# Kernel optimization log

Hardware: AMD Instinct MI355X
Metric: run time of the kernel (lower is better)

The kernel has to match this reference:

```python
import jax, jax.numpy as jnp
import numpy as np

B, K, D = 4096, 100, 64          # batch, multi_factor*top_k, emb_dim
NU, NI = 100000, 50000           # n_users, n_items
MLP_DIMS = [2 * K, K, K // 2, 25, 12, 1]  # 200,100,50,25,12,1


def setup_inputs() -> dict:
    key = jax.random.key(0)
    ks = jax.random.split(key, 30)
    inp = {
        "user_idxs": jax.random.randint(ks[0], (B,), 0, NU),
        "item_idxs": jax.random.randint(ks[1], (B,), 0, NI),
        "user_idx_tensor": jax.random.randint(ks[2], (NU, K), 0, NU),
        "item_idx_tensor": jax.random.randint(ks[3], (NI, K), 0, NI),
        "user_scr_tensor": jax.random.uniform(ks[4], (NU, K), dtype=jnp.float32),
        "item_scr_tensor": jax.random.uniform(ks[5], (NI, K), dtype=jnp.float32),
        "user_emb": jax.random.normal(ks[6], (NU, D), dtype=jnp.float32),
        "item_emb": jax.random.normal(ks[7], (NI, D), dtype=jnp.float32),
    }
    i = 8
    for net in ("n1", "n2"):
        for li, (a, b) in enumerate(zip(MLP_DIMS[:-1], MLP_DIMS[1:]), 1):
            lim = 1.0 / np.sqrt(a)
            inp[f"{net}_w{li}"] = jax.random.uniform(ks[i], (a, b), minval=-lim, maxval=lim, dtype=jnp.float32); i += 1
            inp[f"{net}_b{li}"] = jax.random.uniform(ks[i], (b,), minval=-lim, maxval=lim, dtype=jnp.float32); i += 1
    return inp


def _mlp(x, ws, bs):
    for w, b in zip(ws[:-1], bs[:-1]):
        x = jax.nn.relu(x @ w + b)
    return x @ ws[-1] + bs[-1]


def reference(user_idxs, item_idxs, user_idx_tensor, item_idx_tensor,
              user_scr_tensor, item_scr_tensor, user_emb, item_emb,
              n1_w1, n1_b1, n1_w2, n1_b2, n1_w3, n1_b3, n1_w4, n1_b4, n1_w5, n1_b5,
              n2_w1, n2_b1, n2_w2, n2_b2, n2_w3, n2_b3, n2_w4, n2_b4, n2_w5, n2_b5):
    # neighbor gather: [B,K,D] embeddings and [B,K] scores
    u_e = user_emb[user_idx_tensor[user_idxs]]
    u_s = user_scr_tensor[user_idxs]
    i_e = item_emb[item_idx_tensor[item_idxs]]
    i_s = item_scr_tensor[item_idxs]
    # torch bmm(emb [B,K,D], score[:,None,:].repeat(1,D,1) [B,D,K]) -> [B,K,K];
    # since the repeated score matrix has identical rows, result = emb.sum(-1) (x) score
    su = u_e.sum(-1)[:, :, None] * u_s[:, None, :]  # [B,K,K]
    si = i_e.sum(-1)[:, :, None] * i_s[:, None, :]  # [B,K,K]
    # cat(dim=1).permute(0,2,1) == cat of transposes along last dim
    x1 = jnp.concatenate([su.transpose(0, 2, 1), si.transpose(0, 2, 1)], axis=2)  # [B,K,2K]
    x2 = jnp.concatenate([su, si], axis=2)                                        # [B,K,2K]
    ws1 = [n1_w1, n1_w2, n1_w3, n1_w4, n1_w5]; bs1 = [n1_b1, n1_b2, n1_b3, n1_b4, n1_b5]
    ws2 = [n2_w1, n2_w2, n2_w3, n2_w4, n2_w5]; bs2 = [n2_b1, n2_b2, n2_b3, n2_b4, n2_b5]
    c1 = _mlp(x1, ws1, bs1)[..., 0]  # [B,K]
    c2 = _mlp(x2, ws2, bs2)[..., 0]  # [B,K]
    return jax.nn.sigmoid(jnp.mean(c1 + c2, axis=1))  # [B]
```

## Files before the change

kernel.cpp:

```cpp
#include <hip/hip_runtime.h>
#include <math.h>

#define KDIM 100
#define DDIM 64

typedef __bf16 bf16x8 __attribute__((ext_vector_type(8)));
typedef float  f32x4  __attribute__((ext_vector_type(4)));
typedef float  f32x2  __attribute__((ext_vector_type(2)));
typedef unsigned int u32;
typedef u32 u32x2 __attribute__((ext_vector_type(2)));

struct Weights {
  const float *w1, *b1, *w2, *b2, *w3, *b3, *w4, *b4, *w5, *b5;
};

__device__ __forceinline__ f32x2 vmax2(f32x2 a, f32x2 b) {
#if __has_builtin(__builtin_elementwise_max)
  return __builtin_elementwise_max(a, b);
#else
  return (f32x2){fmaxf(a[0], b[0]), fmaxf(a[1], b[1])};
#endif
}

constexpr int L_VEC  = 0;
constexpr int L_PA   = 400;
constexpr int L_TAIL = 912;
constexpr int L_C    = 1424;
constexpr int SM_F   = 1680;
constexpr int H2T_BYTE = SM_F * 4;
constexpr int H3T_BYTE = H2T_BYTE + 4 * 2048;
constexpr int SM_BYTES = H3T_BYTE + 4 * 1024;

__global__ void prep_kernel(const float* __restrict__ user_emb,
                            const float* __restrict__ item_emb,
                            float* __restrict__ u_rowsum,
                            float* __restrict__ i_rowsum,
                            int NU, int NI, Weights N1, Weights N2,
                            __bf16* __restrict__ wfrag, float* __restrict__ tail) {
  const int tid  = threadIdx.x;
  const int lane = tid & 63;
  const int g = lane >> 4, c16 = lane & 15;
  const int gw = (blockIdx.x * blockDim.x + tid) >> 6;

  if (gw < 42) {
    const int net = gw / 21, f = gw % 21;
    const Weights W = net ? N2 : N1;
    bf16x8 v;
    if (f < 16) {
      const int mt = f >> 2, ks = f & 3;
      #pragma unroll
      for (int i = 0; i < 8; ++i) {
        const int k = 32 * ks + 8 * g + i, m = 16 * mt + c16;
        v[i] = (__bf16)((k < 100 && m < 50) ? W.w2[k * 50 + m] : 0.f);
      }
    } else if (f < 20) {
      const int mt = (f - 16) >> 1, ks = (f - 16) & 1;
      #pragma unroll
      for (int i = 0; i < 8; ++i) {
        const int k = 32 * ks + 8 * g + i, m = 16 * mt + c16;
        v[i] = (__bf16)((k < 50 && m < 25) ? W.w3[k * 25 + m] : 0.f);
      }
    } else {
      #pragma unroll
      for (int i = 0; i < 8; ++i) {
        const int k = 8 * g + i, m = c16;
        v[i] = (__bf16)((k < 25 && m < 12) ? W.w4[k * 12 + m] : 0.f);
      }
    }
    *(bf16x8*)(wfrag + (size_t)gw * 512 + lane * 8) = v;
  }

  if (blockIdx.x == 0) {
    for (int e = tid; e < 512; e += 256) {
      float v;
      if (e < 256)      { const int j = e & 127; const Weights W = (e & 128) ? N2 : N1; v = (j < 100) ? W.b1[j] : 0.f; }
      else if (e < 384) { const int t = e - 256; const int j = t & 63; const Weights W = (t & 64) ? N2 : N1; v = (j < 50) ? W.b2[j] : 0.f; }
      else if (e < 448) { const int t = e - 384; const int j = t & 31; const Weights W = (t & 32) ? N2 : N1; v = (j < 25) ? W.b3[j] : 0.f; }
      else if (e < 480) { const int t = e - 448; const int j = t & 15; const Weights W = (t & 16) ? N2 : N1; v = (j < 12) ? W.b4[j] : 0.f; }
      else              { const int t = e - 480; const int j = t & 15; const Weights W = (t & 16) ? N2 : N1; v = (j < 12) ? W.w5[j] : 0.f; }
      tail[e] = v;
    }
  }

  const int NR = NU + NI;
  const int chunk = lane & 15, lrow = lane >> 4;
  const int nwave = (gridDim.x * blockDim.x) >> 6;
  for (int base = gw * 4; base < NR; base += nwave * 4) {
    const int r = base + lrow;
    float s = 0.f;
    if (r < NR) {
      const float* src = (r < NU) ? (user_emb + (size_t)r * DDIM)
                                  : (item_emb + (size_t)(r - NU) * DDIM);
      const float4 v4 = ((const float4*)src)[chunk];
      s = v4.x + v4.y + v4.z + v4.w;
    }
    s += __shfl_xor(s, 1); s += __shfl_xor(s, 2);
    s += __shfl_xor(s, 4); s += __shfl_xor(s, 8);
    if (chunk == 0 && r < NR) {
      if (r < NU) u_rowsum[r] = s; else i_rowsum[r - NU] = s;
    }
  }
}

__global__ void __launch_bounds__(256) proj_kernel(
    const int* __restrict__ user_idxs, const int* __restrict__ item_idxs,
    const int* __restrict__ uidx_t, const int* __restrict__ iidx_t,
    const float* __restrict__ uscr, const float* __restrict__ iscr,
    const float* __restrict__ u_rowsum, const float* __restrict__ i_rowsum,
    const float* __restrict__ n1w1, const float* __restrict__ n2w1,
    float* __restrict__ VG, float* __restrict__ PAG, int B)
{
  __shared__ float VT[100][20];
  __shared__ float W1S[50][128];
  __shared__ int sidx[16];
  const int tid = threadIdx.x;
  const int sel = blockIdx.x & 3;
  const int b0  = (blockIdx.x >> 2) * 16;

  if (tid < 16) {
    const int b = b0 + tid;
    const int bb = (b < B) ? b : (B - 1);
    sidx[tid] = (sel & 1) ? item_idxs[bb] : user_idxs[bb];
  }
  __syncthreads();

  {
    const int bl = tid >> 4, strip = tid & 15;
    const size_t row = (size_t)sidx[bl] * KDIM;
    if (sel < 2) {
      const int* it = (sel == 0) ? uidx_t : iidx_t;
      const float* rs = (sel == 0) ? u_rowsum : i_rowsum;
      int idxs[7];
      #pragma unroll
      for (int i = 0; i < 7; ++i) {
        const int k = strip + 16 * i;
        idxs[i] = (k < KDIM) ? it[row + k] : 0;
      }
      #pragma unroll
      for (int i = 0; i < 7; ++i) {
        const int k = strip + 16 * i;
        if (k < KDIM) VT[k][bl] = rs[idxs[i]];
      }
    } else {
      const float* sc = (sel == 2) ? uscr : iscr;
      #pragma unroll
      for (int i = 0; i < 7; ++i) {
        const int k = strip + 16 * i;
        if (k < KDIM) VT[k][bl] = sc[row + k];
      }
    }
  }

  const float* w1 = (sel < 2) ? n1w1 : n2w1;
  const int rb = (sel & 1) * KDIM;
  const int jg = tid & 31, bg = tid >> 5;
  float acc[2][4];
  #pragma unroll
  for (int bi = 0; bi < 2; ++bi)
    #pragma unroll
    for (int ji = 0; ji < 4; ++ji) acc[bi][ji] = 0.f;

  for (int kh = 0; kh < 2; ++kh) {
    __syncthreads();
    for (int e = tid; e < 1600; e += 256) {
      const int k = e >> 5, s = e & 31;
      float4 v;
      if (s < 25) v = ((const float4*)(w1 + (size_t)(rb + kh * 50 + k) * KDIM))[s];
      else        v = make_float4(0.f, 0.f, 0.f, 0.f);
      *(float4*)&W1S[k][4 * s] = v;
    }
    __syncthreads();
    #pragma unroll 2
    for (int k = 0; k < 50; ++k) {
      const f32x2 v = *(const f32x2*)&VT[kh * 50 + k][2 * bg];
      const float4 w = *(const float4*)&W1S[k][4 * jg];
      const float ww[4] = {w.x, w.y, w.z, w.w};
      #pragma unroll
      for (int ji = 0; ji < 4; ++ji) {
        acc[0][ji] = fmaf(v[0], ww[ji], acc[0][ji]);
        acc[1][ji] = fmaf(v[1], ww[ji], acc[1][ji]);
      }
    }
  }

  #pragma unroll
  for (int bi = 0; bi < 2; ++bi) {
    const int b = b0 + 2 * bg + bi;
    if (b < B) {
      float4 o = make_float4(acc[bi][0], acc[bi][1], acc[bi][2], acc[bi][3]);
      *(float4*)(PAG + ((size_t)sel * B + b) * 128 + 4 * jg) = o;
    }
  }
  {
    const int bl = tid >> 4, strip = tid & 15;
    const int b = b0 + bl;
    if (b < B) {
      float* dst = VG + ((size_t)sel * B + b) * KDIM;
      #pragma unroll
      for (int i = 0; i < 7; ++i) {
        const int k = strip + 16 * i;
        if (k < KDIM) dst[k] = VT[k][bl];
      }
    }
  }
}

__global__ void __launch_bounds__(256, 4) mlp_kernel(
    const float* __restrict__ VG, const float* __restrict__ PAG,
    const float* __restrict__ tail,
    const float* __restrict__ n1b5, const float* __restrict__ n2b5,
    const __bf16* __restrict__ wfrag, float* __restrict__ out, int B)
{
  __shared__ __align__(16) char smem[SM_BYTES];
  float* sm = (float*)smem;
  const int tid  = threadIdx.x;
  const int lane = tid & 63;
  const int wv   = tid >> 6;
  const int g    = lane >> 4;
  const int c16  = lane & 15;
  const int b    = blockIdx.x;
  const f32x2 Z2 = {0.f, 0.f};

  if (tid < 128) {
    const int sel = tid >> 5, s = tid & 31;
    *(float4*)&sm[L_PA + sel * 128 + 4 * s] =
        *(const float4*)(PAG + ((size_t)sel * B + b) * 128 + 4 * s);
  } else {
    const int t = tid - 128;
    *(float4*)&sm[L_TAIL + 4 * t] = *(const float4*)(tail + 4 * t);
  }
  if (tid < 200) {
    const int sel = tid / 50, r = tid % 50;
    *(f32x2*)&sm[L_VEC + sel * 100 + 2 * r] =
        *(const f32x2*)(VG + ((size_t)sel * B + b) * KDIM + 2 * r);
  }
  __syncthreads();

  const int net = wv >> 1;
  const int qp  = wv & 1;
  const int vA  = net ? (L_VEC + 0)   : (L_VEC + 200);
  const int vB  = net ? (L_VEC + 100) : (L_VEC + 300);
  const int pAo = L_PA + net * 256;
  const int pBo = pAo + 128;
  const char* wfb = (const char*)wfrag + net * 21 * 1024;
  char* h2t = smem + H2T_BYTE + wv * 2048;
  char* h3t = smem + H3T_BYTE + wv * 1024;
  const float b5v = net ? n2b5[0] : n1b5[0];
  const int t7 = c16 & 7, t3 = c16 & 3;

  for (int qq = 0; qq < 2; ++qq) {
    const int q  = 2 * qp + qq;
    const int r0 = 25 * q;

    float sAr[2], sBr[2];
    #pragma unroll
    for (int c = 0; c < 2; ++c) {
      const int row = r0 + 16 * c + c16;
      const int rr = row < KDIM ? row : (KDIM - 1);
      sAr[c] = sm[vA + rr]; sBr[c] = sm[vB + rr];
    }

    f32x4 acc2[2][4];
    #pragma unroll
    for (int c = 0; c < 2; ++c)
      #pragma unroll
      for (int mt = 0; mt < 4; ++mt) acc2[c][mt] = (f32x4){0.f, 0.f, 0.f, 0.f};

    #pragma unroll
    for (int ks = 0; ks < 4; ++ks) {
      const int jb = 32 * ks + 8 * g;
      const f32x2* pa2 = (const f32x2*)&sm[pAo + jb];
      const f32x2* pb2 = (const f32x2*)&sm[pBo + jb];
      const f32x2* b12 = (const f32x2*)&sm[L_TAIL + net * 128 + jb];
      f32x2 paf[4], pbf[4], b1f[4];
      #pragma unroll
      for (int i = 0; i < 4; ++i) { paf[i] = pa2[i]; pbf[i] = pb2[i]; b1f[i] = b12[i]; }
      bf16x8 hb[2];
      #pragma unroll
      for (int c = 0; c < 2; ++c) {
        const f32x2 sa = {sAr[c], sAr[c]}, sb = {sBr[c], sBr[c]};
        bf16x8 a;
        #pragma unroll
        for (int i2 = 0; i2 < 4; ++i2) {
          f32x2 t = sb * pbf[i2] + b1f[i2];
          t = sa * paf[i2] + t;
          t = vmax2(t, Z2);
          a[2 * i2]     = (__bf16)t[0];
          a[2 * i2 + 1] = (__bf16)t[1];
        }
        hb[c] = a;
      }
      __builtin_amdgcn_s_setprio(1);
      #pragma unroll
      for (int mt = 0; mt < 4; ++mt) {
        const bf16x8 a = *(const bf16x8*)(wfb + (mt * 4 + ks) * 1024 + lane * 16);
        acc2[0][mt] = __builtin_amdgcn_mfma_f32_16x16x32_bf16(a, hb[0], acc2[0][mt], 0, 0, 0);
        acc2[1][mt] = __builtin_amdgcn_mfma_f32_16x16x32_bf16(a, hb[1], acc2[1][mt], 0, 0, 0);
      }
      __builtin_amdgcn_s_setprio(0);
    }

    #pragma unroll
    for (int c = 0; c < 2; ++c) {
      #pragma unroll
      for (int mt = 0; mt < 4; ++mt) {
        const f32x2* b2p = (const f32x2*)&sm[L_TAIL + 256 + net * 64 + 16 * mt + 4 * g];
        const f32x4 x = acc2[c][mt];
        const f32x2 lo = vmax2((f32x2){x[0], x[1]} + b2p[0], Z2);
        const f32x2 hi = vmax2((f32x2){x[2], x[3]} + b2p[1], Z2);
        union { __bf16 e[4]; u32x2 w; } o;
        o.e[0] = (__bf16)lo[0]; o.e[1] = (__bf16)lo[1];
        o.e[2] = (__bf16)hi[0]; o.e[3] = (__bf16)hi[1];
        const int S = (2 * mt + (g >> 1)) ^ t7;
        *(u32x2*)(h2t + c16 * 128 + S * 16 + (g & 1) * 8) = o.w;
      }

      f32x4 acc3[2];
      #pragma unroll
      for (int mt = 0; mt < 2; ++mt) acc3[mt] = (f32x4){0.f, 0.f, 0.f, 0.f};
      #pragma unroll
      for (int ks = 0; ks < 2; ++ks) {
        const int S = (4 * ks + g) ^ t7;
        const bf16x8 hbf = *(const bf16x8*)(h2t + c16 * 128 + S * 16);
        __builtin_amdgcn_s_setprio(1);
        #pragma unroll
        for (int mt = 0; mt < 2; ++mt) {
          const bf16x8 a = *(const bf16x8*)(wfb + (16 + mt * 2 + ks) * 1024 + lane * 16);
          acc3[mt] = __builtin_amdgcn_mfma_f32_16x16x32_bf16(a, hbf, acc3[mt], 0, 0, 0);
        }
        __builtin_amdgcn_s_setprio(0);
      }
      #pragma unroll
      for (int mt = 0; mt < 2; ++mt) {
        const f32x2* b3p = (const f32x2*)&sm[L_TAIL + 384 + net * 32 + 16 * mt + 4 * g];
        const f32x4 x = acc3[mt];
        const f32x2 lo = vmax2((f32x2){x[0], x[1]} + b3p[0], Z2);
        const f32x2 hi = vmax2((f32x2){x[2], x[3]} + b3p[1], Z2);
        union { __bf16 e[4]; u32x2 w; } o;
        o.e[0] = (__bf16)lo[0]; o.e[1] = (__bf16)lo[1];
        o.e[2] = (__bf16)hi[0]; o.e[3] = (__bf16)hi[1];
        const int S = (2 * mt + (g >> 1)) ^ t3;
        *(u32x2*)(h3t + c16 * 64 + S * 16 + (g & 1) * 8) = o.w;
      }

      {
        const int S = g ^ t3;
        const bf16x8 hbf = *(const bf16x8*)(h3t + c16 * 64 + S * 16);
        const bf16x8 a = *(const bf16x8*)(wfb + 20 * 1024 + lane * 16);
        const f32x4 z = {0.f, 0.f, 0.f, 0.f};
        __builtin_amdgcn_s_setprio(1);
        const f32x4 acc4 = __builtin_amdgcn_mfma_f32_16x16x32_bf16(a, hbf, z, 0, 0, 0);
        __builtin_amdgcn_s_setprio(0);
        const f32x2* b4p = (const f32x2*)&sm[L_TAIL + 448 + net * 16 + 4 * g];
        const f32x2* w5p = (const f32x2*)&sm[L_TAIL + 480 + net * 16 + 4 * g];
        const f32x2 lo = vmax2((f32x2){acc4[0], acc4[1]} + b4p[0], Z2);
        const f32x2 hi = vmax2((f32x2){acc4[2], acc4[3]} + b4p[1], Z2);
        float v = lo[0] * w5p[0][0] + lo[1] * w5p[0][1]
                + hi[0] * w5p[1][0] + hi[1] * w5p[1][1];
        v += __shfl_xor(v, 16); v += __shfl_xor(v, 32);
        const int lr = 16 * c + c16;
        if (g == 0 && lr < 25)
          sm[L_C + net * 128 + r0 + lr] = v + b5v;
      }
    }
  }
  __syncthreads();

  float v = 0.f;
  if (tid < KDIM) v = sm[L_C + tid] + sm[L_C + 128 + tid];
  if (tid < 128) {
    #pragma unroll
    for (int d = 1; d < 64; d <<= 1) v += __shfl_xor(v, d);
    if ((tid & 63) == 0) sm[tid >> 6] = v;
  }
  __syncthreads();
  if (tid == 0) out[b] = 1.f / (1.f + expf(-0.01f * (sm[0] + sm[1])));
}

extern "C" void kernel_launch(void* const* d_in, const int* in_sizes, int n_in,
                              void* d_out, int out_size, void* d_ws, size_t ws_size,
                              hipStream_t stream) {
  const int*   user_idxs = (const int*)d_in[0];
  const int*   item_idxs = (const int*)d_in[1];
  const int*   uidx_t    = (const int*)d_in[2];
  const int*   iidx_t    = (const int*)d_in[3];
  const float* uscr      = (const float*)d_in[4];
  const float* iscr      = (const float*)d_in[5];
  const float* uemb      = (const float*)d_in[6];
  const float* iemb      = (const float*)d_in[7];

  const int B  = in_sizes[0];
  const int NU = in_sizes[6] / DDIM;
  const int NI = in_sizes[7] / DDIM;

  Weights N1 { (const float*)d_in[8],  (const float*)d_in[9],
               (const float*)d_in[10], (const float*)d_in[11],
               (const float*)d_in[12], (const float*)d_in[13],
               (const float*)d_in[14], (const float*)d_in[15],
               (const float*)d_in[16], (const float*)d_in[17] };
  Weights N2 { (const float*)d_in[18], (const float*)d_in[19],
               (const float*)d_in[20], (const float*)d_in[21],
               (const float*)d_in[22], (const float*)d_in[23],
               (const float*)d_in[24], (const float*)d_in[25],
               (const float*)d_in[26], (const float*)d_in[27] };

  char* ws = (char*)d_ws;
  float* u_rowsum = (float*)ws;
  float* i_rowsum = u_rowsum + NU;
  size_t off = (((size_t)(NU + NI) * 4 + 1023) & ~(size_t)1023);
  __bf16* wfrag = (__bf16*)(ws + off);
  float*  tail  = (float*)(wfrag + (size_t)42 * 512);
  off += (((size_t)42 * 512 * 2 + 512 * 4 + 1023) & ~(size_t)1023);
  float* VG  = (float*)(ws + off);
  off += (size_t)4 * B * KDIM * 4;
  float* PAG = (float*)(ws + off);

  float* out = (float*)d_out;

  prep_kernel<<<1024, 256, 0, stream>>>(uemb, iemb, u_rowsum, i_rowsum, NU, NI, N1, N2, wfrag, tail);
  const int nbt = (B + 15) / 16;
  proj_kernel<<<nbt * 4, 256, 0, stream>>>(user_idxs, item_idxs, uidx_t, iidx_t,
                                           uscr, iscr, u_rowsum, i_rowsum,
                                           N1.w1, N2.w1, VG, PAG, B);
  mlp_kernel<<<B, 256, 0, stream>>>(VG, PAG, tail, N1.b5, N2.b5, wfrag, out, B);
}
```

Before: 76.84 us.

## Interleave both row-quarters per wave to expose more independent MFMA chains

Each wave now processes its two 25-row quarters together instead of one after the other. Layer-1 MFMAs for both quarters share each weight fragment load, and layers 2-4 run with doubled per-wave LDS scratch so two independent MFMA chains are in flight. The goal is to hide MFMA and LDS latency and amortise weight-fragment loads. In exchange it needs more registers (launch bounds lowered from 4 to 3 blocks per CU) and more LDS, which reduces occupancy.

```diff
diff --git a/kernel.cpp b/kernel.cpp
--- a/kernel.cpp
+++ b/kernel.cpp
@@ -28,8 +28,8 @@
 constexpr int L_C    = 1424;
 constexpr int SM_F   = 1680;
 constexpr int H2T_BYTE = SM_F * 4;
-constexpr int H3T_BYTE = H2T_BYTE + 4 * 2048;
-constexpr int SM_BYTES = H3T_BYTE + 4 * 1024;
+constexpr int H3T_BYTE = H2T_BYTE + 8 * 2048;
+constexpr int SM_BYTES = H3T_BYTE + 8 * 1024;
 
 __global__ void prep_kernel(const float* __restrict__ user_emb,
                             const float* __restrict__ item_emb,
@@ -205,7 +205,7 @@
   }
 }
 
-__global__ void __launch_bounds__(256, 4) mlp_kernel(
+__global__ void __launch_bounds__(256, 3) mlp_kernel(
     const float* __restrict__ VG, const float* __restrict__ PAG,
     const float* __restrict__ tail,
     const float* __restrict__ n1b5, const float* __restrict__ n2b5,
@@ -243,42 +243,46 @@
   const int pAo = L_PA + net * 256;
   const int pBo = pAo + 128;
   const char* wfb = (const char*)wfrag + net * 21 * 1024;
-  char* h2t = smem + H2T_BYTE + wv * 2048;
-  char* h3t = smem + H3T_BYTE + wv * 1024;
+  char* h2t0 = smem + H2T_BYTE + (wv * 2 + 0) * 2048;
+  char* h2t1 = smem + H2T_BYTE + (wv * 2 + 1) * 2048;
+  char* h3t0 = smem + H3T_BYTE + (wv * 2 + 0) * 1024;
+  char* h3t1 = smem + H3T_BYTE + (wv * 2 + 1) * 1024;
   const float b5v = net ? n2b5[0] : n1b5[0];
   const int t7 = c16 & 7, t3 = c16 & 3;
 
-  for (int qq = 0; qq < 2; ++qq) {
-    const int q  = 2 * qp + qq;
-    const int r0 = 25 * q;
-
-    float sAr[2], sBr[2];
+  float sAr[2][2], sBr[2][2];
+  #pragma unroll
+  for (int qt = 0; qt < 2; ++qt)
     #pragma unroll
     for (int c = 0; c < 2; ++c) {
-      const int row = r0 + 16 * c + c16;
+      const int row = 25 * (2 * qp + qt) + 16 * c + c16;
       const int rr = row < KDIM ? row : (KDIM - 1);
-      sAr[c] = sm[vA + rr]; sBr[c] = sm[vB + rr];
-    }
-
-    f32x4 acc2[2][4];
+      sAr[qt][c] = sm[vA + rr]; sBr[qt][c] = sm[vB + rr];
+    }
+
+  f32x4 acc2[2][2][4];
+  #pragma unroll
+  for (int qt = 0; qt < 2; ++qt)
     #pragma unroll
     for (int c = 0; c < 2; ++c)
       #pragma unroll
-      for (int mt = 0; mt < 4; ++mt) acc2[c][mt] = (f32x4){0.f, 0.f, 0.f, 0.f};
-
-    #pragma unroll
-    for (int ks = 0; ks < 4; ++ks) {
-      const int jb = 32 * ks + 8 * g;
-      const f32x2* pa2 = (const f32x2*)&sm[pAo + jb];
-      const f32x2* pb2 = (const f32x2*)&sm[pBo + jb];
-      const f32x2* b12 = (const f32x2*)&sm[L_TAIL + net * 128 + jb];
-      f32x2 paf[4], pbf[4], b1f[4];
-      #pragma unroll
-      for (int i = 0; i < 4; ++i) { paf[i] = pa2[i]; pbf[i] = pb2[i]; b1f[i] = b12[i]; }
-      bf16x8 hb[2];
+      for (int mt = 0; mt < 4; ++mt) acc2[qt][c][mt] = (f32x4){0.f, 0.f, 0.f, 0.f};
+
+  #pragma unroll
+  for (int ks = 0; ks < 4; ++ks) {
+    const int jb = 32 * ks + 8 * g;
+    const f32x2* pa2 = (const f32x2*)&sm[pAo + jb];
+    const f32x2* pb2 = (const f32x2*)&sm[pBo + jb];
+    const f32x2* b12 = (const f32x2*)&sm[L_TAIL + net * 128 + jb];
+    f32x2 paf[4], pbf[4], b1f[4];
+    #pragma unroll
+    for (int i = 0; i < 4; ++i) { paf[i] = pa2[i]; pbf[i] = pb2[i]; b1f[i] = b12[i]; }
+    bf16x8 hb[2][2];
+    #pragma unroll
+    for (int qt = 0; qt < 2; ++qt)
       #pragma unroll
       for (int c = 0; c < 2; ++c) {
-        const f32x2 sa = {sAr[c], sAr[c]}, sb = {sBr[c], sBr[c]};
+        const f32x2 sa = {sAr[qt][c], sAr[qt][c]}, sb = {sBr[qt][c], sBr[qt][c]};
         bf16x8 a;
         #pragma unroll
         for (int i2 = 0; i2 < 4; ++i2) {
@@ -288,24 +292,30 @@
           a[2 * i2]     = (__bf16)t[0];
           a[2 * i2 + 1] = (__bf16)t[1];
         }
-        hb[c] = a;
-      }
-      __builtin_amdgcn_s_setprio(1);
-      #pragma unroll
-      for (int mt = 0; mt < 4; ++mt) {
-        const bf16x8 a = *(const bf16x8*)(wfb + (mt * 4 + ks) * 1024 + lane * 16);
-        acc2[0][mt] = __builtin_amdgcn_mfma_f32_16x16x32_bf16(a, hb[0], acc2[0][mt], 0, 0, 0);
-        acc2[1][mt] = __builtin_amdgcn_mfma_f32_16x16x32_bf16(a, hb[1], acc2[1][mt], 0, 0, 0);
-      }
-      __builtin_amdgcn_s_setprio(0);
-    }
-
-    #pragma unroll
-    for (int c = 0; c < 2; ++c) {
+        hb[qt][c] = a;
+      }
+    __builtin_amdgcn_s_setprio(1);
+    #pragma unroll
+    for (int mt = 0; mt < 4; ++mt) {
+      const bf16x8 a = *(const bf16x8*)(wfb + (mt * 4 + ks) * 1024 + lane * 16);
+      #pragma unroll
+      for (int qt = 0; qt < 2; ++qt) {
+        acc2[qt][0][mt] = __builtin_amdgcn_mfma_f32_16x16x32_bf16(a, hb[qt][0], acc2[qt][0][mt], 0, 0, 0);
+        acc2[qt][1][mt] = __builtin_amdgcn_mfma_f32_16x16x32_bf16(a, hb[qt][1], acc2[qt][1][mt], 0, 0, 0);
+      }
+    }
+    __builtin_amdgcn_s_setprio(0);
+  }
+
+  #pragma unroll
+  for (int c = 0; c < 2; ++c) {
+    #pragma unroll
+    for (int qt = 0; qt < 2; ++qt) {
+      char* h2t = qt ? h2t1 : h2t0;
       #pragma unroll
       for (int mt = 0; mt < 4; ++mt) {
         const f32x2* b2p = (const f32x2*)&sm[L_TAIL + 256 + net * 64 + 16 * mt + 4 * g];
-        const f32x4 x = acc2[c][mt];
+        const f32x4 x = acc2[qt][c][mt];
         const f32x2 lo = vmax2((f32x2){x[0], x[1]} + b2p[0], Z2);
         const f32x2 hi = vmax2((f32x2){x[2], x[3]} + b2p[1], Z2);
         union { __bf16 e[4]; u32x2 w; } o;
@@ -314,26 +324,34 @@
         const int S = (2 * mt + (g >> 1)) ^ t7;
         *(u32x2*)(h2t + c16 * 128 + S * 16 + (g & 1) * 8) = o.w;
       }
-
-      f32x4 acc3[2];
-      #pragma unroll
-      for (int mt = 0; mt < 2; ++mt) acc3[mt] = (f32x4){0.f, 0.f, 0.f, 0.f};
-      #pragma unroll
-      for (int ks = 0; ks < 2; ++ks) {
-        const int S = (4 * ks + g) ^ t7;
-        const bf16x8 hbf = *(const bf16x8*)(h2t + c16 * 128 + S * 16);
-        __builtin_amdgcn_s_setprio(1);
-        #pragma unroll
-        for (int mt = 0; mt < 2; ++mt) {
-          const bf16x8 a = *(const bf16x8*)(wfb + (16 + mt * 2 + ks) * 1024 + lane * 16);
-          acc3[mt] = __builtin_amdgcn_mfma_f32_16x16x32_bf16(a, hbf, acc3[mt], 0, 0, 0);
-        }
-        __builtin_amdgcn_s_setprio(0);
-      }
+    }
+
+    f32x4 acc3[2][2];
+    #pragma unroll
+    for (int qt = 0; qt < 2; ++qt)
+      #pragma unroll
+      for (int mt = 0; mt < 2; ++mt) acc3[qt][mt] = (f32x4){0.f, 0.f, 0.f, 0.f};
+    #pragma unroll
+    for (int ks = 0; ks < 2; ++ks) {
+      const int S = (4 * ks + g) ^ t7;
+      const bf16x8 hbf0 = *(const bf16x8*)(h2t0 + c16 * 128 + S * 16);
+      const bf16x8 hbf1 = *(const bf16x8*)(h2t1 + c16 * 128 + S * 16);
+      __builtin_amdgcn_s_setprio(1);
+      #pragma unroll
+      for (int mt = 0; mt < 2; ++mt) {
+        const bf16x8 a = *(const bf16x8*)(wfb + (16 + mt * 2 + ks) * 1024 + lane * 16);
+        acc3[0][mt] = __builtin_amdgcn_mfma_f32_16x16x32_bf16(a, hbf0, acc3[0][mt], 0, 0, 0);
+        acc3[1][mt] = __builtin_amdgcn_mfma_f32_16x16x32_bf16(a, hbf1, acc3[1][mt], 0, 0, 0);
+      }
+      __builtin_amdgcn_s_setprio(0);
+    }
+    #pragma unroll
+    for (int qt = 0; qt < 2; ++qt) {
+      char* h3t = qt ? h3t1 : h3t0;
       #pragma unroll
       for (int mt = 0; mt < 2; ++mt) {
         const f32x2* b3p = (const f32x2*)&sm[L_TAIL + 384 + net * 32 + 16 * mt + 4 * g];
-        const f32x4 x = acc3[mt];
+        const f32x4 x = acc3[qt][mt];
         const f32x2 lo = vmax2((f32x2){x[0], x[1]} + b3p[0], Z2);
         const f32x2 hi = vmax2((f32x2){x[2], x[3]} + b3p[1], Z2);
         union { __bf16 e[4]; u32x2 w; } o;
@@ -342,25 +360,31 @@
         const int S = (2 * mt + (g >> 1)) ^ t3;
         *(u32x2*)(h3t + c16 * 64 + S * 16 + (g & 1) * 8) = o.w;
       }
-
-      {
-        const int S = g ^ t3;
-        const bf16x8 hbf = *(const bf16x8*)(h3t + c16 * 64 + S * 16);
-        const bf16x8 a = *(const bf16x8*)(wfb + 20 * 1024 + lane * 16);
-        const f32x4 z = {0.f, 0.f, 0.f, 0.f};
-        __builtin_amdgcn_s_setprio(1);
-        const f32x4 acc4 = __builtin_amdgcn_mfma_f32_16x16x32_bf16(a, hbf, z, 0, 0, 0);
-        __builtin_amdgcn_s_setprio(0);
-        const f32x2* b4p = (const f32x2*)&sm[L_TAIL + 448 + net * 16 + 4 * g];
-        const f32x2* w5p = (const f32x2*)&sm[L_TAIL + 480 + net * 16 + 4 * g];
-        const f32x2 lo = vmax2((f32x2){acc4[0], acc4[1]} + b4p[0], Z2);
-        const f32x2 hi = vmax2((f32x2){acc4[2], acc4[3]} + b4p[1], Z2);
+    }
+
+    {
+      const int S = g ^ t3;
+      const bf16x8 hbf0 = *(const bf16x8*)(h3t0 + c16 * 64 + S * 16);
+      const bf16x8 hbf1 = *(const bf16x8*)(h3t1 + c16 * 64 + S * 16);
+      const bf16x8 a = *(const bf16x8*)(wfb + 20 * 1024 + lane * 16);
+      const f32x4 z = {0.f, 0.f, 0.f, 0.f};
+      __builtin_amdgcn_s_setprio(1);
+      const f32x4 acc4_0 = __builtin_amdgcn_mfma_f32_16x16x32_bf16(a, hbf0, z, 0, 0, 0);
+      const f32x4 acc4_1 = __builtin_amdgcn_mfma_f32_16x16x32_bf16(a, hbf1, z, 0, 0, 0);
+      __builtin_amdgcn_s_setprio(0);
+      const f32x2* b4p = (const f32x2*)&sm[L_TAIL + 448 + net * 16 + 4 * g];
+      const f32x2* w5p = (const f32x2*)&sm[L_TAIL + 480 + net * 16 + 4 * g];
+      #pragma unroll
+      for (int qt = 0; qt < 2; ++qt) {
+        const f32x4 x = qt ? acc4_1 : acc4_0;
+        const f32x2 lo = vmax2((f32x2){x[0], x[1]} + b4p[0], Z2);
+        const f32x2 hi = vmax2((f32x2){x[2], x[3]} + b4p[1], Z2);
         float v = lo[0] * w5p[0][0] + lo[1] * w5p[0][1]
                 + hi[0] * w5p[1][0] + hi[1] * w5p[1][1];
         v += __shfl_xor(v, 16); v += __shfl_xor(v, 32);
         const int lr = 16 * c + c16;
         if (g == 0 && lr < 25)
-          sm[L_C + net * 128 + r0 + lr] = v + b5v;
+          sm[L_C + net * 128 + 25 * (2 * qp + qt) + lr] = v + b5v;
       }
     }
   }
```

After: 76.18 us. No clear change (-0.9%).
